# Performance work log

Hardware: AMD Instinct MI355X
Metric: run time of the kernel (lower is better)

Reference implementation:

```python
import math
import jax, jax.numpy as jnp
import numpy as np

B, T, C = 2, 2048, 1024
H, Ca = 16, 64


def setup_inputs() -> dict:
    key = jax.random.key(0)
    ks = jax.random.split(key, 5)
    # kaiming-uniform-ish scale for weights
    wb = 1.0 / math.sqrt(C)
    return {
        "x": jax.random.normal(ks[0], (B, T, C), dtype=jnp.float32),
        "w_q": jax.random.uniform(ks[1], (H, C, Ca), jnp.float32, -wb, wb),
        "w_k": jax.random.uniform(ks[2], (H, C, Ca), jnp.float32, -wb, wb),
        "w_v": jax.random.uniform(ks[3], (H, C, Ca), jnp.float32, -wb, wb),
        "w_o": jax.random.uniform(ks[4], (C, C), jnp.float32, -wb, wb),
    }


def reference(x, w_q, w_k, w_v, w_o):
    # x: [B,T,C]; w_q/w_k/w_v: [H,C,Ca]; w_o: [C,C]
    scale = 1.0 / math.sqrt(w_q.shape[-1])
    q = jnp.einsum("btc,hca->bhta", x, w_q)  # [B,H,T,Ca]
    k = jnp.einsum("btc,hca->bhta", x, w_k)
    v = jnp.einsum("btc,hca->bhta", x, w_v)
    s = jnp.einsum("bhta,bhsa->bhts", q, k)  # [B,H,T,T]
    # faithful to original: mask where tril(s)==0, scale applied after masking
    s_hat = jnp.where(jnp.tril(s) == 0, -jnp.inf, s * scale)
    a = jax.nn.softmax(s_hat, axis=-1)
    y = jnp.einsum("bhts,bhsa->bhta", a, v)  # [B,H,T,Ca]
    y_cat = y.transpose(0, 2, 1, 3).reshape(x.shape)  # [B,T,C]
    return y_cat @ w_o
```

## Files before the change

kernel.cpp:

```cpp
#include <hip/hip_runtime.h>
#include <stdint.h>

#define Bc 2
#define Tc 2048
#define Cn 1024
#define Hc 16
#define CAc 64

typedef __attribute__((ext_vector_type(8))) short short8;
typedef __attribute__((ext_vector_type(4))) float f32x4;

#define QSCALE 0.18033688011112042f

__device__ __forceinline__ unsigned short f2bf(float f) {
    unsigned int u = __builtin_bit_cast(unsigned int, f);
    return (unsigned short)((u + 0x7fffu + ((u >> 16) & 1u)) >> 16);
}
__device__ __forceinline__ unsigned int pack_rne(float a, float b) {
    return (unsigned int)f2bf(a) | ((unsigned int)f2bf(b) << 16);
}
__device__ __forceinline__ unsigned int pack_trunc(float a, float b) {
    return __builtin_amdgcn_perm(__builtin_bit_cast(unsigned int, b),
                                 __builtin_bit_cast(unsigned int, a), 0x07060302u);
}

__device__ __forceinline__ void async_cp16(const unsigned short* g, unsigned short* l) {
    __builtin_amdgcn_global_load_lds(
        (const __attribute__((address_space(1))) unsigned int*)g,
        (__attribute__((address_space(3))) unsigned int*)l,
        16, 0, 0);
}

__device__ __forceinline__ int detect_bf16(const unsigned short* x) {
    int c = 0;
#pragma unroll
    for (int i = 0; i < 64; i++) {
        unsigned short u = x[i * 2];
        int e = (u >> 7) & 0xFF;
        c += (e >= 0x68 && e <= 0x90);
    }
    return c > 32;
}

__device__ __forceinline__ unsigned short ld_elem(const void* base, size_t off, int isbf) {
    return isbf ? ((const unsigned short*)base)[off] : f2bf(((const float*)base)[off]);
}

__global__ __launch_bounds__(256) void prep(
    const void* __restrict__ xin, unsigned short* __restrict__ xb,
    const void* __restrict__ wq, const void* __restrict__ wk,
    const void* __restrict__ wv, const void* __restrict__ wo,
    unsigned short* __restrict__ wT, unsigned short* __restrict__ woT)
{
    const int isbf = detect_bf16((const unsigned short*)xin);
    const int bx = blockIdx.x;
    if (bx < 4096) {
        if (isbf) return;
        int idx = (bx * 256 + threadIdx.x) * 4;
        const float* xf = (const float*)xin;
        float4 v = *(const float4*)(xf + idx);
        uint2 p;
        p.x = pack_rne(v.x, v.y);
        p.y = pack_rne(v.z, v.w);
        *(uint2*)(&xb[idx]) = p;
        return;
    }
    __shared__ unsigned short tile[32][33];
    const int t = threadIdx.x;
    const int tx = t & 31, ty = t >> 5;
    const void* src;
    unsigned short* dst;
    int R, Cw, r0, c0;
    if (bx < 7168) {
        int rem0 = bx - 4096;
        int g = rem0 >> 6;
        int rem = rem0 & 63;
        int ct = rem >> 1;
        int at = rem & 1;
        int proj = g >> 4, h = g & 15;
        const void* wsel = (proj == 0) ? wq : ((proj == 1) ? wk : wv);
        src = isbf ? (const void*)((const unsigned short*)wsel + (size_t)h * Cn * CAc)
                   : (const void*)((const float*)wsel + (size_t)h * Cn * CAc);
        dst = wT + (size_t)g * CAc * Cn;
        R = Cn; Cw = CAc; r0 = ct * 32; c0 = at * 32;
    } else {
        int rem = bx - 7168;
        src = wo; dst = woT;
        R = Cn; Cw = Cn;
        r0 = (rem >> 5) * 32; c0 = (rem & 31) * 32;
    }
#pragma unroll
    for (int j = 0; j < 4; j++)
        tile[ty + j * 8][tx] = ld_elem(src, (size_t)(r0 + ty + j * 8) * Cw + c0 + tx, isbf);
    __syncthreads();
#pragma unroll
    for (int j = 0; j < 4; j++)
        dst[(size_t)(c0 + ty + j * 8) * R + r0 + tx] = tile[tx][ty + j * 8];
}

__global__ __launch_bounds__(256) void gemm_qkv(
    const void* __restrict__ xin,
    const unsigned short* __restrict__ xb,
    const unsigned short* __restrict__ Bt,
    unsigned short* __restrict__ o0,
    unsigned short* __restrict__ o1,
    unsigned short* __restrict__ o2)
{
    __shared__ alignas(16) unsigned short SH[4][128 * 32];
    const int tid = threadIdx.x;
    const int wave = tid >> 6, lane = tid & 63;
    const int l15 = lane & 15, quad = lane >> 4;
    const int mBase = blockIdx.y * 128, nBase = blockIdx.x * 128;
    const int mOff = (wave & 1) * 64, nOff = (wave >> 1) * 64;

    const int isbf = detect_bf16((const unsigned short*)xin);
    const unsigned short* Amat = isbf ? (const unsigned short*)xin : xb;

    const int srow = lane >> 2;
    const int sgc  = (lane & 3) ^ (srow & 3);
    const int sw = (quad ^ (l15 & 3)) * 8;

    f32x4 acc[4][4];
#pragma unroll
    for (int i = 0; i < 4; i++)
#pragma unroll
        for (int j = 0; j < 4; j++)
            acc[i][j] = (f32x4){0.f, 0.f, 0.f, 0.f};

#pragma unroll
    for (int t = 0; t < 2; t++) {
        int rl = wave * 32 + t * 16;
        async_cp16(Amat + (size_t)(mBase + rl + srow) * Cn + sgc * 8, &SH[0][rl * 32]);
        async_cp16(Bt   + (size_t)(nBase + rl + srow) * Cn + sgc * 8, &SH[2][rl * 32]);
    }
    __syncthreads();

    for (int kk = 0; kk < 32; kk++) {
        const int cur = kk & 1;
        if (kk < 31) {
            const int k1 = (kk + 1) * 32;
#pragma unroll
            for (int t = 0; t < 2; t++) {
                int rl = wave * 32 + t * 16;
                async_cp16(Amat + (size_t)(mBase + rl + srow) * Cn + k1 + sgc * 8, &SH[1 - cur][rl * 32]);
                async_cp16(Bt   + (size_t)(nBase + rl + srow) * Cn + k1 + sgc * 8, &SH[3 - cur][rl * 32]);
            }
        }
        short8 af[4], bfr[4];
#pragma unroll
        for (int i = 0; i < 4; i++)
            af[i] = *(const short8*)(&SH[cur][(mOff + i * 16 + l15) * 32 + sw]);
#pragma unroll
        for (int j = 0; j < 4; j++)
            bfr[j] = *(const short8*)(&SH[2 + cur][(nOff + j * 16 + l15) * 32 + sw]);
#pragma unroll
        for (int i = 0; i < 4; i++)
#pragma unroll
            for (int j = 0; j < 4; j++)
                acc[i][j] = __builtin_amdgcn_mfma_f32_16x16x32_bf16(af[i], bfr[j], acc[i][j], 0, 0, 0);
        __syncthreads();
    }

    const int bb = mBase >> 11;
    if (nBase < 2048) {
        const float sc = (nBase < 1024) ? QSCALE : 1.0f;
        unsigned short* dst = (nBase < 1024) ? o0 : o1;
#pragma unroll
        for (int i = 0; i < 4; i++) {
            int m0 = mBase + mOff + i * 16 + quad * 4;
            int t0 = m0 & (Tc - 1);
#pragma unroll
            for (int j = 0; j < 4; j++) {
                int n = nBase + nOff + j * 16 + l15;
                int h = (n >> 6) & 15, a = n & 63;
                size_t base = ((size_t)(bb * Hc + h) * Tc + t0) * CAc + a;
#pragma unroll
                for (int r = 0; r < 4; r++)
                    dst[base + (size_t)r * CAc] = f2bf(acc[i][j][r] * sc);
            }
        }
    } else {
        unsigned short* Cl = &SH[0][0];
#pragma unroll
        for (int i = 0; i < 4; i++) {
            int c16 = (mOff >> 3) + i * 2 + (quad >> 1);
            int p = quad & 1;
#pragma unroll
            for (int j = 0; j < 4; j++) {
                int nl = nOff + j * 16 + l15;
                int cs = c16 ^ (nl & 7);
                uint2 v8;
                v8.x = pack_rne(acc[i][j][0], acc[i][j][1]);
                v8.y = pack_rne(acc[i][j][2], acc[i][j][3]);
                *(uint2*)(&Cl[nl * 128 + cs * 8 + p * 4]) = v8;
            }
        }
        __syncthreads();
        const int tLoc = mBase & (Tc - 1);
#pragma unroll
        for (int pp = 0; pp < 8; pp++) {
            int vr = pp * 16 + wave * 4 + (lane >> 4);
            int cc = lane & 15;
            int cs = cc ^ (vr & 7);
            uint4 val = *(const uint4*)(&Cl[vr * 128 + cs * 8]);
            int n = nBase + vr;
            int hh = (n >> 6) & 15, a = n & 63;
            *(uint4*)(&o2[((size_t)(bb * Hc + hh) * CAc + a) * Tc + tLoc + cc * 8]) = val;
        }
    }
}

__global__ __launch_bounds__(256) void gemm_out(
    const unsigned short* __restrict__ Amat,
    const unsigned short* __restrict__ Bt,
    void* __restrict__ o0,
    const void* __restrict__ xin)
{
    __shared__ alignas(16) unsigned short Al[2][64 * 32];
    __shared__ alignas(16) unsigned short Bl[2][128 * 32];
    const int tid = threadIdx.x;
    const int wave = tid >> 6, lane = tid & 63;
    const int l15 = lane & 15, quad = lane >> 4;
    const int mBase = blockIdx.y * 64, nBase = blockIdx.x * 128;
    const int mOff = (wave & 1) * 32, nOff = (wave >> 1) * 64;

    const int isbf = detect_bf16((const unsigned short*)xin);

    const int srow = lane >> 2;
    const int sgc  = (lane & 3) ^ (srow & 3);
    const int sw = (quad ^ (l15 & 3)) * 8;

    f32x4 acc[2][4];
#pragma unroll
    for (int i = 0; i < 2; i++)
#pragma unroll
        for (int j = 0; j < 4; j++)
            acc[i][j] = (f32x4){0.f, 0.f, 0.f, 0.f};

    {
        int rlA = wave * 16;
        async_cp16(Amat + (size_t)(mBase + rlA + srow) * Cn + sgc * 8, &Al[0][rlA * 32]);
#pragma unroll
        for (int t = 0; t < 2; t++) {
            int rlB = wave * 32 + t * 16;
            async_cp16(Bt + (size_t)(nBase + rlB + srow) * Cn + sgc * 8, &Bl[0][rlB * 32]);
        }
    }
    __syncthreads();

    for (int kk = 0; kk < 32; kk++) {
        const int cur = kk & 1;
        if (kk < 31) {
            const int k1 = (kk + 1) * 32;
            int rlA = wave * 16;
            async_cp16(Amat + (size_t)(mBase + rlA + srow) * Cn + k1 + sgc * 8, &Al[1 - cur][rlA * 32]);
#pragma unroll
            for (int t = 0; t < 2; t++) {
                int rlB = wave * 32 + t * 16;
                async_cp16(Bt + (size_t)(nBase + rlB + srow) * Cn + k1 + sgc * 8, &Bl[1 - cur][rlB * 32]);
            }
        }
        short8 af[2], bfr[4];
#pragma unroll
        for (int i = 0; i < 2; i++)
            af[i] = *(const short8*)(&Al[cur][(mOff + i * 16 + l15) * 32 + sw]);
#pragma unroll
        for (int j = 0; j < 4; j++)
            bfr[j] = *(const short8*)(&Bl[cur][(nOff + j * 16 + l15) * 32 + sw]);
#pragma unroll
        for (int i = 0; i < 2; i++)
#pragma unroll
            for (int j = 0; j < 4; j++)
                acc[i][j] = __builtin_amdgcn_mfma_f32_16x16x32_bf16(af[i], bfr[j], acc[i][j], 0, 0, 0);
        __syncthreads();
    }

#pragma unroll
    for (int i = 0; i < 2; i++) {
        int m0 = mBase + mOff + i * 16 + quad * 4;
#pragma unroll
        for (int j = 0; j < 4; j++) {
            int n = nBase + nOff + j * 16 + l15;
            if (isbf) {
#pragma unroll
                for (int r = 0; r < 4; r++)
                    ((unsigned short*)o0)[(size_t)(m0 + r) * Cn + n] = f2bf(acc[i][j][r]);
            } else {
#pragma unroll
                for (int r = 0; r < 4; r++)
                    ((float*)o0)[(size_t)(m0 + r) * Cn + n] = acc[i][j][r];
            }
        }
    }
}

__global__ __launch_bounds__(256) void attn_pair(
    const unsigned short* __restrict__ q,
    const unsigned short* __restrict__ k,
    const unsigned short* __restrict__ vT,
    unsigned short* __restrict__ y)
{
    __shared__ alignas(16) unsigned short Kl[2][64 * 64];
    __shared__ alignas(16) unsigned short Vl[2][64 * 64];
    const int LDP = 72;
    __shared__ alignas(16) unsigned short Pl[4][16 * LDP];
    const int bx = blockIdx.x;
    const int pr = bx & 15, bh = bx >> 4;
    const int h = bh & 15, b = bh >> 4;
    const int qt1 = pr, qt2 = 31 - pr;
    const int tid = threadIdx.x;
    const int wave = tid >> 6, lane = tid & 63;
    const int l15 = lane & 15, quad = lane >> 4;
    const int m0w1 = qt1 * 64 + wave * 16;
    const int m0w2 = qt2 * 64 + wave * 16;
    const size_t bhoff = (size_t)(b * Hc + h);
    const unsigned short* qh = q + bhoff * Tc * CAc;
    const unsigned short* kh = k + bhoff * Tc * CAc;
    const unsigned short* vh = vT + bhoff * CAc * Tc;

    const int srow = (lane >> 3);
    const int sgc  = (lane & 7) ^ srow;
    const int h7 = l15 & 7;
    const int sw0 = ((quad ^ h7) << 3);
    const int sw1 = (((4 + quad) ^ h7) << 3);

    short8 qf1[2], qf2[2];
#pragma unroll
    for (int s = 0; s < 2; s++) {
        qf1[s] = *(const short8*)(&qh[(size_t)(m0w1 + l15) * CAc + s * 32 + quad * 8]);
        qf2[s] = *(const short8*)(&qh[(size_t)(m0w2 + l15) * CAc + s * 32 + quad * 8]);
    }

    f32x4 oacc1[4], oacc2[4], osum1, osum2;
#pragma unroll
    for (int j2 = 0; j2 < 4; j2++) {
        oacc1[j2] = (f32x4){0.f, 0.f, 0.f, 0.f};
        oacc2[j2] = (f32x4){0.f, 0.f, 0.f, 0.f};
    }
    osum1 = (f32x4){0.f, 0.f, 0.f, 0.f};
    osum2 = (f32x4){0.f, 0.f, 0.f, 0.f};

    const unsigned short ONE = 0x3F80;
    short8 ones;
#pragma unroll
    for (int i = 0; i < 8; i++) ones[i] = (short)ONE;

    unsigned short* Pw = &Pl[wave][0];

#pragma unroll
    for (int t = 0; t < 2; t++) {
        int rl = wave * 16 + t * 8;
        async_cp16(kh + (size_t)(rl + srow) * CAc + sgc * 8, &Kl[0][rl * 64]);
        async_cp16(vh + (size_t)(rl + srow) * Tc  + sgc * 8, &Vl[0][rl * 64]);
    }
    __syncthreads();

    for (int kt = 0; kt <= qt2; kt++) {
        const int k0 = kt * 64;
        const int cur = kt & 1;
        const bool act1 = (kt <= qt1);
        if (kt < qt2) {
            const unsigned short* kg = kh + (size_t)(k0 + 64) * CAc;
            const unsigned short* vg = vh + (k0 + 64);
#pragma unroll
            for (int t = 0; t < 2; t++) {
                int rl = wave * 16 + t * 8;
                async_cp16(kg + (size_t)(rl + srow) * CAc + sgc * 8, &Kl[1 - cur][rl * 64]);
                async_cp16(vg + (size_t)(rl + srow) * Tc  + sgc * 8, &Vl[1 - cur][rl * 64]);
            }
        }
        const unsigned short* Kc = Kl[cur];
        const unsigned short* Vc = Vl[cur];

        float s1[4][4], s2[4][4];
#pragma unroll
        for (int j = 0; j < 4; j++) {
            short8 kf0 = *(const short8*)(&Kc[(j * 16 + l15) * 64 + sw0]);
            short8 kf1 = *(const short8*)(&Kc[(j * 16 + l15) * 64 + sw1]);
            f32x4 z2 = (f32x4){0.f, 0.f, 0.f, 0.f};
            z2 = __builtin_amdgcn_mfma_f32_16x16x32_bf16(kf0, qf2[0], z2, 0, 0, 0);
            z2 = __builtin_amdgcn_mfma_f32_16x16x32_bf16(kf1, qf2[1], z2, 0, 0, 0);
#pragma unroll
            for (int r = 0; r < 4; r++) s2[j][r] = z2[r];
            if (act1) {
                f32x4 z1 = (f32x4){0.f, 0.f, 0.f, 0.f};
                z1 = __builtin_amdgcn_mfma_f32_16x16x32_bf16(kf0, qf1[0], z1, 0, 0, 0);
                z1 = __builtin_amdgcn_mfma_f32_16x16x32_bf16(kf1, qf1[1], z1, 0, 0, 0);
#pragma unroll
                for (int r = 0; r < 4; r++) s1[j][r] = z1[r];
            }
        }

        if (kt == qt2) {
            int tg = m0w2 + l15;
#pragma unroll
            for (int j = 0; j < 4; j++)
#pragma unroll
                for (int r = 0; r < 4; r++) {
                    int sg = k0 + j * 16 + quad * 4 + r;
                    s2[j][r] = (sg <= tg) ? exp2f(s2[j][r]) : 0.f;
                }
        } else {
#pragma unroll
            for (int j = 0; j < 4; j++)
#pragma unroll
                for (int r = 0; r < 4; r++)
                    s2[j][r] = exp2f(s2[j][r]);
        }
        if (act1) {
            if (kt == qt1) {
                int tg = m0w1 + l15;
#pragma unroll
                for (int j = 0; j < 4; j++)
#pragma unroll
                    for (int r = 0; r < 4; r++) {
                        int sg = k0 + j * 16 + quad * 4 + r;
                        s1[j][r] = (sg <= tg) ? exp2f(s1[j][r]) : 0.f;
                    }
            } else {
#pragma unroll
                for (int j = 0; j < 4; j++)
#pragma unroll
                    for (int r = 0; r < 4; r++)
                        s1[j][r] = exp2f(s1[j][r]);
            }
        }

        short8 pa2[2], pa1[2];
#pragma unroll
        for (int j = 0; j < 4; j++) {
            uint2 v;
            v.x = pack_trunc(s2[j][0], s2[j][1]);
            v.y = pack_trunc(s2[j][2], s2[j][3]);
            *(uint2*)(&Pw[l15 * LDP + j * 16 + quad * 4]) = v;
        }
#pragma unroll
        for (int c = 0; c < 2; c++)
            pa2[c] = *(const short8*)(&Pw[l15 * LDP + c * 32 + quad * 8]);
        if (act1) {
#pragma unroll
            for (int j = 0; j < 4; j++) {
                uint2 v;
                v.x = pack_trunc(s1[j][0], s1[j][1]);
                v.y = pack_trunc(s1[j][2], s1[j][3]);
                *(uint2*)(&Pw[l15 * LDP + j * 16 + quad * 4]) = v;
            }
#pragma unroll
            for (int c = 0; c < 2; c++)
                pa1[c] = *(const short8*)(&Pw[l15 * LDP + c * 32 + quad * 8]);
        }

#pragma unroll
        for (int c = 0; c < 2; c++) {
#pragma unroll
            for (int j2 = 0; j2 < 4; j2++) {
                short8 vb = *(const short8*)(&Vc[(j2 * 16 + l15) * 64 + (c ? sw1 : sw0)]);
                oacc2[j2] = __builtin_amdgcn_mfma_f32_16x16x32_bf16(pa2[c], vb, oacc2[j2], 0, 0, 0);
                if (act1)
                    oacc1[j2] = __builtin_amdgcn_mfma_f32_16x16x32_bf16(pa1[c], vb, oacc1[j2], 0, 0, 0);
            }
            osum2 = __builtin_amdgcn_mfma_f32_16x16x32_bf16(pa2[c], ones, osum2, 0, 0, 0);
            if (act1)
                osum1 = __builtin_amdgcn_mfma_f32_16x16x32_bf16(pa1[c], ones, osum1, 0, 0, 0);
        }
        __syncthreads();
    }

    float ri1[4], ri2[4];
#pragma unroll
    for (int r = 0; r < 4; r++) { ri1[r] = 1.0f / osum1[r]; ri2[r] = 1.0f / osum2[r]; }
#pragma unroll
    for (int j2 = 0; j2 < 4; j2++) {
#pragma unroll
        for (int r = 0; r < 4; r++) {
            int t1 = m0w1 + quad * 4 + r;
            int t2 = m0w2 + quad * 4 + r;
            y[((size_t)b * Tc + t1) * Cn + h * CAc + j2 * 16 + l15] = f2bf(oacc1[j2][r] * ri1[r]);
            y[((size_t)b * Tc + t2) * Cn + h * CAc + j2 * 16 + l15] = f2bf(oacc2[j2][r] * ri2[r]);
        }
    }
}

extern "C" void kernel_launch(void* const* d_in, const int* in_sizes, int n_in,
                              void* d_out, int out_size, void* d_ws, size_t ws_size,
                              hipStream_t stream) {
    const void* x  = d_in[0];
    const void* wq = d_in[1];
    const void* wk = d_in[2];
    const void* wv = d_in[3];
    const void* wo = d_in[4];
    char* ws = (char*)d_ws;
    unsigned short* wT  = (unsigned short*)(ws + ((size_t)1 << 20));
    unsigned short* woT = (unsigned short*)(ws + ((size_t)7 << 20));
    unsigned short* xb  = (unsigned short*)(ws + ((size_t)9 << 20));
    unsigned short* qb  = (unsigned short*)(ws + ((size_t)17 << 20));
    unsigned short* kb  = (unsigned short*)(ws + ((size_t)25 << 20));
    unsigned short* vTb = (unsigned short*)(ws + ((size_t)33 << 20));
    unsigned short* yb  = (unsigned short*)(ws + ((size_t)41 << 20));

    prep<<<dim3(8192), dim3(256), 0, stream>>>(x, xb, wq, wk, wv, wo, wT, woT);
    gemm_qkv<<<dim3(24, 32), dim3(256), 0, stream>>>(x, xb, wT, qb, kb, vTb);
    attn_pair<<<dim3(512), dim3(256), 0, stream>>>(qb, kb, vTb, yb);
    gemm_out<<<dim3(8, 64), dim3(256), 0, stream>>>(yb, woT, d_out, x);
}
```

Baseline: 206.6 us.

## Split paired-tile attention into one query tile per block, longest first

The attention kernel previously handled two query tiles per block (a short and a long causal tile) so that every block had balanced work. Now each block processes a single 64-row query tile, with blocks ordered longest-first, and the grid grows from 512 to 1024 blocks under a launch bound that asks for 4 blocks per SIMD. The P staging buffer switches from a padded row stride to an XOR swizzle, and exp2f is replaced by the hardware exp2 builtin. This trades the paired load balancing for more parallelism and lower register pressure, but each block reloads K/V for its own tile, so K/V traffic rises.

```diff
diff --git a/kernel.cpp b/kernel.cpp
--- a/kernel.cpp
+++ b/kernel.cpp
@@ -294,7 +294,7 @@
     }
 }
 
-__global__ __launch_bounds__(256) void attn_pair(
+__global__ __launch_bounds__(256, 4) void attn_t(
     const unsigned short* __restrict__ q,
     const unsigned short* __restrict__ k,
     const unsigned short* __restrict__ vT,
@@ -302,17 +302,15 @@
 {
     __shared__ alignas(16) unsigned short Kl[2][64 * 64];
     __shared__ alignas(16) unsigned short Vl[2][64 * 64];
-    const int LDP = 72;
-    __shared__ alignas(16) unsigned short Pl[4][16 * LDP];
+    __shared__ alignas(16) unsigned short Pl[4][16 * 64];
     const int bx = blockIdx.x;
-    const int pr = bx & 15, bh = bx >> 4;
+    const int qt = 31 - (bx >> 5);
+    const int bh = bx & 31;
     const int h = bh & 15, b = bh >> 4;
-    const int qt1 = pr, qt2 = 31 - pr;
     const int tid = threadIdx.x;
     const int wave = tid >> 6, lane = tid & 63;
     const int l15 = lane & 15, quad = lane >> 4;
-    const int m0w1 = qt1 * 64 + wave * 16;
-    const int m0w2 = qt2 * 64 + wave * 16;
+    const int m0w = qt * 64 + wave * 16;
     const size_t bhoff = (size_t)(b * Hc + h);
     const unsigned short* qh = q + bhoff * Tc * CAc;
     const unsigned short* kh = k + bhoff * Tc * CAc;
@@ -323,22 +321,17 @@
     const int h7 = l15 & 7;
     const int sw0 = ((quad ^ h7) << 3);
     const int sw1 = (((4 + quad) ^ h7) << 3);
-
-    short8 qf1[2], qf2[2];
-#pragma unroll
-    for (int s = 0; s < 2; s++) {
-        qf1[s] = *(const short8*)(&qh[(size_t)(m0w1 + l15) * CAc + s * 32 + quad * 8]);
-        qf2[s] = *(const short8*)(&qh[(size_t)(m0w2 + l15) * CAc + s * 32 + quad * 8]);
-    }
-
-    f32x4 oacc1[4], oacc2[4], osum1, osum2;
-#pragma unroll
-    for (int j2 = 0; j2 < 4; j2++) {
-        oacc1[j2] = (f32x4){0.f, 0.f, 0.f, 0.f};
-        oacc2[j2] = (f32x4){0.f, 0.f, 0.f, 0.f};
-    }
-    osum1 = (f32x4){0.f, 0.f, 0.f, 0.f};
-    osum2 = (f32x4){0.f, 0.f, 0.f, 0.f};
+    const int pw_m = 2 * h7;
+
+    short8 qf[2];
+#pragma unroll
+    for (int s = 0; s < 2; s++)
+        qf[s] = *(const short8*)(&qh[(size_t)(m0w + l15) * CAc + s * 32 + quad * 8]);
+
+    f32x4 oacc[4], osum;
+#pragma unroll
+    for (int j2 = 0; j2 < 4; j2++) oacc[j2] = (f32x4){0.f, 0.f, 0.f, 0.f};
+    osum = (f32x4){0.f, 0.f, 0.f, 0.f};
 
     const unsigned short ONE = 0x3F80;
     short8 ones;
@@ -355,11 +348,10 @@
     }
     __syncthreads();
 
-    for (int kt = 0; kt <= qt2; kt++) {
+    for (int kt = 0; kt <= qt; kt++) {
         const int k0 = kt * 64;
         const int cur = kt & 1;
-        const bool act1 = (kt <= qt1);
-        if (kt < qt2) {
+        if (kt < qt) {
             const unsigned short* kg = kh + (size_t)(k0 + 64) * CAc;
             const unsigned short* vg = vh + (k0 + 64);
 #pragma unroll
@@ -372,111 +364,68 @@
         const unsigned short* Kc = Kl[cur];
         const unsigned short* Vc = Vl[cur];
 
-        float s1[4][4], s2[4][4];
+        float sv[4][4];
 #pragma unroll
         for (int j = 0; j < 4; j++) {
             short8 kf0 = *(const short8*)(&Kc[(j * 16 + l15) * 64 + sw0]);
             short8 kf1 = *(const short8*)(&Kc[(j * 16 + l15) * 64 + sw1]);
-            f32x4 z2 = (f32x4){0.f, 0.f, 0.f, 0.f};
-            z2 = __builtin_amdgcn_mfma_f32_16x16x32_bf16(kf0, qf2[0], z2, 0, 0, 0);
-            z2 = __builtin_amdgcn_mfma_f32_16x16x32_bf16(kf1, qf2[1], z2, 0, 0, 0);
-#pragma unroll
-            for (int r = 0; r < 4; r++) s2[j][r] = z2[r];
-            if (act1) {
-                f32x4 z1 = (f32x4){0.f, 0.f, 0.f, 0.f};
-                z1 = __builtin_amdgcn_mfma_f32_16x16x32_bf16(kf0, qf1[0], z1, 0, 0, 0);
-                z1 = __builtin_amdgcn_mfma_f32_16x16x32_bf16(kf1, qf1[1], z1, 0, 0, 0);
-#pragma unroll
-                for (int r = 0; r < 4; r++) s1[j][r] = z1[r];
-            }
-        }
-
-        if (kt == qt2) {
-            int tg = m0w2 + l15;
+            f32x4 z = (f32x4){0.f, 0.f, 0.f, 0.f};
+            z = __builtin_amdgcn_mfma_f32_16x16x32_bf16(kf0, qf[0], z, 0, 0, 0);
+            z = __builtin_amdgcn_mfma_f32_16x16x32_bf16(kf1, qf[1], z, 0, 0, 0);
+#pragma unroll
+            for (int r = 0; r < 4; r++) sv[j][r] = z[r];
+        }
+
+        if (kt == qt) {
+            int tg = m0w + l15;
 #pragma unroll
             for (int j = 0; j < 4; j++)
 #pragma unroll
                 for (int r = 0; r < 4; r++) {
                     int sg = k0 + j * 16 + quad * 4 + r;
-                    s2[j][r] = (sg <= tg) ? exp2f(s2[j][r]) : 0.f;
+                    sv[j][r] = (sg <= tg) ? __builtin_amdgcn_exp2f(sv[j][r]) : 0.f;
                 }
         } else {
 #pragma unroll
             for (int j = 0; j < 4; j++)
 #pragma unroll
                 for (int r = 0; r < 4; r++)
-                    s2[j][r] = exp2f(s2[j][r]);
-        }
-        if (act1) {
-            if (kt == qt1) {
-                int tg = m0w1 + l15;
-#pragma unroll
-                for (int j = 0; j < 4; j++)
-#pragma unroll
-                    for (int r = 0; r < 4; r++) {
-                        int sg = k0 + j * 16 + quad * 4 + r;
-                        s1[j][r] = (sg <= tg) ? exp2f(s1[j][r]) : 0.f;
-                    }
-            } else {
-#pragma unroll
-                for (int j = 0; j < 4; j++)
-#pragma unroll
-                    for (int r = 0; r < 4; r++)
-                        s1[j][r] = exp2f(s1[j][r]);
-            }
-        }
-
-        short8 pa2[2], pa1[2];
+                    sv[j][r] = __builtin_amdgcn_exp2f(sv[j][r]);
+        }
+
+        short8 pa[2];
 #pragma unroll
         for (int j = 0; j < 4; j++) {
             uint2 v;
-            v.x = pack_trunc(s2[j][0], s2[j][1]);
-            v.y = pack_trunc(s2[j][2], s2[j][3]);
-            *(uint2*)(&Pw[l15 * LDP + j * 16 + quad * 4]) = v;
+            v.x = pack_trunc(sv[j][0], sv[j][1]);
+            v.y = pack_trunc(sv[j][2], sv[j][3]);
+            *(uint2*)(&Pw[l15 * 64 + ((j * 4 + quad) ^ pw_m) * 4]) = v;
         }
 #pragma unroll
         for (int c = 0; c < 2; c++)
-            pa2[c] = *(const short8*)(&Pw[l15 * LDP + c * 32 + quad * 8]);
-        if (act1) {
-#pragma unroll
-            for (int j = 0; j < 4; j++) {
-                uint2 v;
-                v.x = pack_trunc(s1[j][0], s1[j][1]);
-                v.y = pack_trunc(s1[j][2], s1[j][3]);
-                *(uint2*)(&Pw[l15 * LDP + j * 16 + quad * 4]) = v;
-            }
-#pragma unroll
-            for (int c = 0; c < 2; c++)
-                pa1[c] = *(const short8*)(&Pw[l15 * LDP + c * 32 + quad * 8]);
-        }
+            pa[c] = *(const short8*)(&Pw[l15 * 64 + ((c * 4 + quad) ^ h7) * 8]);
 
 #pragma unroll
         for (int c = 0; c < 2; c++) {
 #pragma unroll
             for (int j2 = 0; j2 < 4; j2++) {
                 short8 vb = *(const short8*)(&Vc[(j2 * 16 + l15) * 64 + (c ? sw1 : sw0)]);
-                oacc2[j2] = __builtin_amdgcn_mfma_f32_16x16x32_bf16(pa2[c], vb, oacc2[j2], 0, 0, 0);
-                if (act1)
-                    oacc1[j2] = __builtin_amdgcn_mfma_f32_16x16x32_bf16(pa1[c], vb, oacc1[j2], 0, 0, 0);
-            }
-            osum2 = __builtin_amdgcn_mfma_f32_16x16x32_bf16(pa2[c], ones, osum2, 0, 0, 0);
-            if (act1)
-                osum1 = __builtin_amdgcn_mfma_f32_16x16x32_bf16(pa1[c], ones, osum1, 0, 0, 0);
+                oacc[j2] = __builtin_amdgcn_mfma_f32_16x16x32_bf16(pa[c], vb, oacc[j2], 0, 0, 0);
+            }
+            osum = __builtin_amdgcn_mfma_f32_16x16x32_bf16(pa[c], ones, osum, 0, 0, 0);
         }
         __syncthreads();
     }
 
-    float ri1[4], ri2[4];
-#pragma unroll
-    for (int r = 0; r < 4; r++) { ri1[r] = 1.0f / osum1[r]; ri2[r] = 1.0f / osum2[r]; }
+    float ri[4];
+#pragma unroll
+    for (int r = 0; r < 4; r++) ri[r] = 1.0f / osum[r];
 #pragma unroll
     for (int j2 = 0; j2 < 4; j2++) {
 #pragma unroll
         for (int r = 0; r < 4; r++) {
-            int t1 = m0w1 + quad * 4 + r;
-            int t2 = m0w2 + quad * 4 + r;
-            y[((size_t)b * Tc + t1) * Cn + h * CAc + j2 * 16 + l15] = f2bf(oacc1[j2][r] * ri1[r]);
-            y[((size_t)b * Tc + t2) * Cn + h * CAc + j2 * 16 + l15] = f2bf(oacc2[j2][r] * ri2[r]);
+            int t = m0w + quad * 4 + r;
+            y[((size_t)b * Tc + t) * Cn + h * CAc + j2 * 16 + l15] = f2bf(oacc[j2][r] * ri[r]);
         }
     }
 }
@@ -500,6 +449,6 @@
 
     prep<<<dim3(8192), dim3(256), 0, stream>>>(x, xb, wq, wk, wv, wo, wT, woT);
     gemm_qkv<<<dim3(24, 32), dim3(256), 0, stream>>>(x, xb, wT, qb, kb, vTb);
-    attn_pair<<<dim3(512), dim3(256), 0, stream>>>(qb, kb, vTb, yb);
+    attn_t<<<dim3(1024), dim3(256), 0, stream>>>(qb, kb, vTb, yb);
     gemm_out<<<dim3(8, 64), dim3(256), 0, stream>>>(yb, woT, d_out, x);
 }
```

Result: faster. 185.3 us (-10.3%).
